# Optimization experiments

Hardware: AMD Instinct MI355X
Metric: run time of the kernel (lower is better)

## Reference

```python
import jax, jax.numpy as jnp
import numpy as np

NUM_HEADS = 12

def setup_inputs() -> dict:
    key = jax.random.key(0)
    ks = jax.random.split(key, 6)
    B, N, C, P = 16, 785, 768, 48
    return {
        "x": jax.random.normal(ks[0], (B, N, C), jnp.float32),
        "qkv_w": jax.random.normal(ks[1], (3 * C, C), jnp.float32) * 0.02,
        "pos_emb": jax.random.normal(ks[2], (N, N, P), jnp.float32) * 0.02,
        "pos_proj_w": jax.random.normal(ks[3], (NUM_HEADS, P), jnp.float32) * 0.02,
        "proj_w": jax.random.normal(ks[4], (C, C), jnp.float32) * 0.02,
        "proj_b": jnp.zeros((C,), jnp.float32),
    }

def reference(x, qkv_w, pos_emb, pos_proj_w, proj_w, proj_b):
    B, N, C = x.shape
    H = NUM_HEADS
    hd = C // H
    scale = hd ** -0.5
    # qkv projection: [B,N,3C] -> q,k,v each [B,H,N,hd]
    qkv = (x @ qkv_w.T).reshape(B, N, 3, H, hd)
    qkv = jnp.transpose(qkv, (2, 0, 3, 1, 4))
    q, k, v = qkv[0], qkv[1], qkv[2]
    # learned relative-position bias: [H,N,N]
    pos_score = jnp.einsum('nmp,hp->hnm', pos_emb, pos_proj_w)
    # attention scores: scale applied AFTER adding bias (matches original)
    attn = (jnp.einsum('bhnd,bhmd->bhnm', q, k) + pos_score[None]) * scale
    attn = jax.nn.softmax(attn, axis=-1)
    out = jnp.einsum('bhnm,bhmd->bhnd', attn, v)
    out = jnp.transpose(out, (0, 2, 1, 3)).reshape(B, N, C)
    return out @ proj_w.T + proj_b
```

## Files before the change

### kernel.cpp

```cpp
#include <hip/hip_runtime.h>
#include <hip/hip_fp16.h>

#define B_ 16
#define N_ 785
#define C_ 768
#define H_ 12
#define HD_ 64
#define P_ 48
#define M_ (B_*N_)
#define POSW 832
#define VTW  832
#define SLOG2E 0.1803368801111244f

#define OFF_Q   0
#define OFF_K   9646080
#define OFF_VT  19292160
#define OFF_POS 29515776
#define OFF_XF  37353216
#define OFF_AO  OFF_XF
#define OFF_WQ  47085312
#define OFF_WP  48854784

struct __align__(16) Half8 { __half h[8]; };
typedef _Float16 half8_t __attribute__((ext_vector_type(8)));
typedef _Float16 half4_t __attribute__((ext_vector_type(4)));
typedef float f32x4 __attribute__((ext_vector_type(4)));

__device__ __forceinline__ void gl16(const void* g, void* l) {
    __builtin_amdgcn_global_load_lds(
        (const __attribute__((address_space(1))) void*)g,
        (__attribute__((address_space(3))) void*)l, 16, 0, 0);
}

#define NX4 2411520
#define NQ4 442368
#define NP4 147456
#define NTOT4 (NX4+NQ4+NP4)

__global__ __launch_bounds__(256) void convert_f16(
    const float* __restrict__ x, const float* __restrict__ wq,
    const float* __restrict__ wp, _Float16* __restrict__ xo,
    _Float16* __restrict__ wqo, _Float16* __restrict__ wpo)
{
    int i = blockIdx.x * 256 + threadIdx.x;
    const float4* s; _Float16* d; int o;
    if (i < NX4)            { s = (const float4*)x;  d = xo;  o = i; }
    else if (i < NX4 + NQ4) { s = (const float4*)wq; d = wqo; o = i - NX4; }
    else                    { s = (const float4*)wp; d = wpo; o = i - NX4 - NQ4; }
    float4 v = s[o];
    half4_t h = { (_Float16)v.x, (_Float16)v.y, (_Float16)v.z, (_Float16)v.w };
    *(half4_t*)&d[o * 4] = h;
}

__global__ __launch_bounds__(256) void qkv_gemm_mfma(
    const _Float16* __restrict__ A, const _Float16* __restrict__ Bw,
    __half* __restrict__ qh, __half* __restrict__ kh, __half* __restrict__ vth)
{
    __shared__ _Float16 Asl[128 * 32];
    __shared__ _Float16 Bsl[128 * 32];

    const int t  = threadIdx.x;
    const int w  = t >> 6;
    const int l  = t & 63;
    const int lr = l & 15;
    const int lg = l >> 4;
    const int wm = (w >> 1) * 64;
    const int wn = (w & 1) * 64;
    const int n0 = blockIdx.x * 128;
    const int m0 = blockIdx.y * 128;

    const int f1 = t + 256;
    const int ar0 = t >> 2,  ac0 = (t & 3) * 8;
    const int ar1 = f1 >> 2, ac1 = (f1 & 3) * 8;
    const _Float16* Ag0 = A  + (size_t)(m0 + ar0) * 768 + ac0;
    const _Float16* Ag1 = A  + (size_t)(m0 + ar1) * 768 + ac1;
    const _Float16* Bg0 = Bw + (size_t)(n0 + ar0) * 768 + ac0;
    const _Float16* Bg1 = Bw + (size_t)(n0 + ar1) * 768 + ac1;
    _Float16* Al0 = &Asl[t * 8];
    _Float16* Al1 = &Asl[f1 * 8];
    _Float16* Bl0 = &Bsl[t * 8];
    _Float16* Bl1 = &Bsl[f1 * 8];

    f32x4 acc[4][4];
    #pragma unroll
    for (int i = 0; i < 4; ++i)
        #pragma unroll
        for (int j = 0; j < 4; ++j) acc[i][j] = (f32x4){0.f, 0.f, 0.f, 0.f};

    for (int k0 = 0; k0 < 768; k0 += 32) {
        gl16(Ag0 + k0, Al0); gl16(Ag1 + k0, Al1);
        gl16(Bg0 + k0, Bl0); gl16(Bg1 + k0, Bl1);
        __syncthreads();
        half8_t af[4], bf[4];
        #pragma unroll
        for (int i = 0; i < 4; ++i)
            af[i] = *(const half8_t*)&Asl[(wm + i * 16 + lr) * 32 + lg * 8];
        #pragma unroll
        for (int j = 0; j < 4; ++j)
            bf[j] = *(const half8_t*)&Bsl[(wn + j * 16 + lr) * 32 + lg * 8];
        __builtin_amdgcn_s_setprio(1);
        #pragma unroll
        for (int i = 0; i < 4; ++i)
            #pragma unroll
            for (int j = 0; j < 4; ++j)
                acc[i][j] = __builtin_amdgcn_mfma_f32_16x16x32_f16(af[i], bf[j], acc[i][j], 0, 0, 0);
        __builtin_amdgcn_s_setprio(0);
        __syncthreads();
    }

    const int tsel  = blockIdx.x / 6;
    const int nbase = n0 - tsel * 768;
    #pragma unroll
    for (int i = 0; i < 4; ++i) {
        #pragma unroll
        for (int r = 0; r < 4; ++r) {
            const int m = m0 + wm + i * 16 + lg * 4 + r;
            if (m >= M_) continue;
            const int bb = m / N_, nn = m - bb * N_;
            #pragma unroll
            for (int j = 0; j < 4; ++j) {
                const int nsec = nbase + wn + j * 16 + lr;
                const int hh = nsec >> 6, dd = nsec & 63;
                const float v = acc[i][j][r];
                if (tsel == 0)
                    qh[((size_t)(bb * H_ + hh) * N_ + nn) * HD_ + dd] = __float2half(v * SLOG2E);
                else if (tsel == 1)
                    kh[((size_t)(bb * H_ + hh) * N_ + nn) * HD_ + dd] = __float2half(v);
                else
                    vth[((size_t)(bb * H_ + hh) * HD_ + dd) * VTW + nn] = __float2half(v);
            }
        }
    }
}

__global__ __launch_bounds__(256) void pos_kernel(
    const float* __restrict__ pe, const float* __restrict__ pw,
    __half* __restrict__ posh)
{
    __shared__ float W[H_][P_];
    const int t = threadIdx.x;
    for (int i = t; i < H_ * P_; i += 256) W[i / P_][i % P_] = pw[i];
    __syncthreads();
    int nm = blockIdx.x * 256 + t;
    if (nm >= N_ * N_) return;
    float e[48];
    const float4* src = (const float4*)(pe + (size_t)nm * 48);
    #pragma unroll
    for (int i = 0; i < 12; ++i) {
        float4 v = src[i];
        e[4*i] = v.x; e[4*i+1] = v.y; e[4*i+2] = v.z; e[4*i+3] = v.w;
    }
    int n = nm / N_, m = nm - n * N_;
    #pragma unroll
    for (int hh = 0; hh < H_; ++hh) {
        float s = 0.f;
        #pragma unroll
        for (int p = 0; p < 48; ++p) s = fmaf(e[p], W[hh][p], s);
        posh[((size_t)hh * N_ + n) * POSW + m] = __float2half(s * SLOG2E);
    }
}

__global__ __launch_bounds__(256) void attn_mfma(
    const _Float16* __restrict__ qh, const _Float16* __restrict__ kh,
    const _Float16* __restrict__ vt, const _Float16* __restrict__ posh,
    _Float16* __restrict__ aoh)
{
    __shared__ _Float16 Kl[64][72];
    __shared__ _Float16 Vl[64][72];
    __shared__ _Float16 Bl[64][72];

    const int t  = threadIdx.x;
    const int w  = t >> 6;
    const int l  = t & 63;
    const int lr = l & 15;
    const int lg = l >> 4;

    const int g   = blockIdx.x;
    const int b   = g & 15;
    const int grp = g >> 4;
    const int qt  = grp / 12;
    const int h   = grp - qt * 12;
    const int bh  = b * H_ + h;
    const int n0  = qt * 64;

    const int qrow = n0 + w * 16 + lr;
    const int qrc  = qrow < N_ ? qrow : N_ - 1;
    const _Float16* qbase = qh + ((size_t)bh * N_ + qrc) * HD_;
    const half8_t qf0 = *(const half8_t*)(qbase + lg * 8);
    const half8_t qf1 = *(const half8_t*)(qbase + 32 + lg * 8);

    f32x4 O0 = {0.f,0.f,0.f,0.f}, O1 = O0, O2 = O0, O3 = O0;
    float m_run = -1e30f;
    float l_run = 0.f;

    const int srow = t >> 2;
    const int scol = (t & 3) * 16;
    const _Float16* kRow = kh + ((size_t)bh * N_) * HD_ + scol;
    const _Float16* vRow = vt + ((size_t)bh * HD_ + srow) * VTW + scol;
    const _Float16* bRow = posh + ((size_t)h * N_ + (n0 + srow < N_ ? n0 + srow : N_ - 1)) * POSW + scol;

    half8_t rk0, rk1, rv0, rv1, rb0, rb1;
    {
        const int gm = srow < N_ ? srow : N_ - 1;
        const half8_t* ks = (const half8_t*)(kRow + (size_t)gm * HD_);
        rk0 = ks[0]; rk1 = ks[1];
        const half8_t* vs = (const half8_t*)vRow;
        rv0 = vs[0]; rv1 = vs[1];
        const half8_t* bs = (const half8_t*)bRow;
        rb0 = bs[0]; rb1 = bs[1];
    }

    for (int c = 0; c < 13; ++c) {
        *(half8_t*)&Kl[srow][scol]     = rk0;
        *(half8_t*)&Kl[srow][scol + 8] = rk1;
        *(half8_t*)&Vl[srow][scol]     = rv0;
        *(half8_t*)&Vl[srow][scol + 8] = rv1;
        *(half8_t*)&Bl[srow][scol]     = rb0;
        *(half8_t*)&Bl[srow][scol + 8] = rb1;
        __syncthreads();

        if (c < 12) {
            const int m0n = (c + 1) * 64;
            const int gm  = (m0n + srow) < N_ ? (m0n + srow) : N_ - 1;
            const half8_t* ks = (const half8_t*)(kRow + (size_t)gm * HD_);
            rk0 = ks[0]; rk1 = ks[1];
            const half8_t* vs = (const half8_t*)(vRow + m0n);
            rv0 = vs[0]; rv1 = vs[1];
            const half8_t* bs = (const half8_t*)(bRow + m0n);
            rb0 = bs[0]; rb1 = bs[1];
        }

        f32x4 s[4];
        __builtin_amdgcn_s_setprio(1);
        #pragma unroll
        for (int ms = 0; ms < 4; ++ms) {
            half8_t k0 = *(const half8_t*)&Kl[ms * 16 + lr][lg * 8];
            half8_t k1 = *(const half8_t*)&Kl[ms * 16 + lr][32 + lg * 8];
            f32x4 acc = {0.f, 0.f, 0.f, 0.f};
            acc = __builtin_amdgcn_mfma_f32_16x16x32_f16(k0, qf0, acc, 0, 0, 0);
            acc = __builtin_amdgcn_mfma_f32_16x16x32_f16(k1, qf1, acc, 0, 0, 0);
            s[ms] = acc;
        }
        __builtin_amdgcn_s_setprio(0);

        #pragma unroll
        for (int ms = 0; ms < 4; ++ms) {
            half4_t b4 = *(const half4_t*)&Bl[w * 16 + lr][ms * 16 + lg * 4];
            s[ms][0] += (float)b4[0];
            s[ms][1] += (float)b4[1];
            s[ms][2] += (float)b4[2];
            s[ms][3] += (float)b4[3];
        }
        if (c == 12) {
            #pragma unroll
            for (int ms = 0; ms < 4; ++ms)
                #pragma unroll
                for (int r = 0; r < 4; ++r)
                    if (ms * 16 + lg * 4 + r >= 17) s[ms][r] = -1e30f;
        }

        float smax = fmaxf(fmaxf(fmaxf(s[0][0], s[0][1]), fmaxf(s[0][2], s[0][3])),
                           fmaxf(fmaxf(s[1][0], s[1][1]), fmaxf(s[1][2], s[1][3])));
        smax = fmaxf(smax, fmaxf(fmaxf(fmaxf(s[2][0], s[2][1]), fmaxf(s[2][2], s[2][3])),
                                 fmaxf(fmaxf(s[3][0], s[3][1]), fmaxf(s[3][2], s[3][3]))));
        smax = fmaxf(smax, __shfl_xor(smax, 16));
        smax = fmaxf(smax, __shfl_xor(smax, 32));

        if (__any(smax > m_run + 8.f)) {
            const float mn    = fmaxf(m_run, smax);
            const float alpha = exp2f(m_run - mn);
            m_run = mn;
            l_run *= alpha;
            const float a0 = __shfl(alpha, lg * 4 + 0);
            const float a1 = __shfl(alpha, lg * 4 + 1);
            const float a2 = __shfl(alpha, lg * 4 + 2);
            const float a3 = __shfl(alpha, lg * 4 + 3);
            O0[0]*=a0; O0[1]*=a1; O0[2]*=a2; O0[3]*=a3;
            O1[0]*=a0; O1[1]*=a1; O1[2]*=a2; O1[3]*=a3;
            O2[0]*=a0; O2[1]*=a1; O2[2]*=a2; O2[3]*=a3;
            O3[0]*=a0; O3[1]*=a1; O3[2]*=a2; O3[3]*=a3;
        }

        float p[4][4];
        float psum = 0.f;
        #pragma unroll
        for (int ms = 0; ms < 4; ++ms)
            #pragma unroll
            for (int r = 0; r < 4; ++r) {
                p[ms][r] = exp2f(s[ms][r] - m_run);
                psum += p[ms][r];
            }
        psum += __shfl_xor(psum, 16);
        psum += __shfl_xor(psum, 32);
        l_run += psum;

        half8_t pa0 = { (_Float16)p[0][0], (_Float16)p[0][1], (_Float16)p[0][2], (_Float16)p[0][3],
                        (_Float16)p[1][0], (_Float16)p[1][1], (_Float16)p[1][2], (_Float16)p[1][3] };
        half8_t pa1 = { (_Float16)p[2][0], (_Float16)p[2][1], (_Float16)p[2][2], (_Float16)p[2][3],
                        (_Float16)p[3][0], (_Float16)p[3][1], (_Float16)p[3][2], (_Float16)p[3][3] };

        __builtin_amdgcn_s_setprio(1);
        #pragma unroll
        for (int ds = 0; ds < 4; ++ds) {
            const _Float16* vr = &Vl[ds * 16 + lr][0];
            half4_t v00 = *(const half4_t*)&vr[lg * 4];
            half4_t v01 = *(const half4_t*)&vr[16 + lg * 4];
            half4_t v10 = *(const half4_t*)&vr[32 + lg * 4];
            half4_t v11 = *(const half4_t*)&vr[48 + lg * 4];
            half8_t vf0 = __builtin_shufflevector(v00, v01, 0, 1, 2, 3, 4, 5, 6, 7);
            half8_t vf1 = __builtin_shufflevector(v10, v11, 0, 1, 2, 3, 4, 5, 6, 7);
            f32x4& Od = (ds == 0 ? O0 : ds == 1 ? O1 : ds == 2 ? O2 : O3);
            Od = __builtin_amdgcn_mfma_f32_16x16x32_f16(pa0, vf0, Od, 0, 0, 0);
            Od = __builtin_amdgcn_mfma_f32_16x16x32_f16(pa1, vf1, Od, 0, 0, 0);
        }
        __builtin_amdgcn_s_setprio(0);
        __syncthreads();
    }

    const int bb = bh / H_;
    #pragma unroll
    for (int r = 0; r < 4; ++r) {
        const int n = n0 + w * 16 + lg * 4 + r;
        if (n >= N_) continue;
        const float lv  = __shfl(l_run, lg * 4 + r);
        const float inv = 1.f / lv;
        _Float16* dst = aoh + ((size_t)(bb * N_ + n)) * C_ + h * HD_;
        dst[0 * 16 + lr] = (_Float16)(O0[r] * inv);
        dst[1 * 16 + lr] = (_Float16)(O1[r] * inv);
        dst[2 * 16 + lr] = (_Float16)(O2[r] * inv);
        dst[3 * 16 + lr] = (_Float16)(O3[r] * inv);
    }
}

__global__ __launch_bounds__(256) void proj_gemm_mfma(
    const _Float16* __restrict__ A, const _Float16* __restrict__ Bw,
    const float* __restrict__ bias, float* __restrict__ out)
{
    __shared__ _Float16 Asl[128 * 32];
    __shared__ _Float16 Bsl[128 * 32];

    const int t  = threadIdx.x;
    const int w  = t >> 6;
    const int l  = t & 63;
    const int lr = l & 15;
    const int lg = l >> 4;
    const int wm = (w >> 1) * 64;
    const int wn = (w & 1) * 64;
    const int n0 = blockIdx.x * 128;
    const int m0 = blockIdx.y * 128;

    const int f1 = t + 256;
    const int ar0 = t >> 2,  ac0 = (t & 3) * 8;
    const int ar1 = f1 >> 2, ac1 = (f1 & 3) * 8;
    const _Float16* Ag0 = A  + (size_t)(m0 + ar0) * 768 + ac0;
    const _Float16* Ag1 = A  + (size_t)(m0 + ar1) * 768 + ac1;
    const _Float16* Bg0 = Bw + (size_t)(n0 + ar0) * 768 + ac0;
    const _Float16* Bg1 = Bw + (size_t)(n0 + ar1) * 768 + ac1;
    _Float16* Al0 = &Asl[t * 8];
    _Float16* Al1 = &Asl[f1 * 8];
    _Float16* Bl0 = &Bsl[t * 8];
    _Float16* Bl1 = &Bsl[f1 * 8];

    f32x4 acc[4][4];
    #pragma unroll
    for (int i = 0; i < 4; ++i)
        #pragma unroll
        for (int j = 0; j < 4; ++j) acc[i][j] = (f32x4){0.f, 0.f, 0.f, 0.f};

    for (int k0 = 0; k0 < 768; k0 += 32) {
        gl16(Ag0 + k0, Al0); gl16(Ag1 + k0, Al1);
        gl16(Bg0 + k0, Bl0); gl16(Bg1 + k0, Bl1);
        __syncthreads();
        half8_t af[4], bf[4];
        #pragma unroll
        for (int i = 0; i < 4; ++i)
            af[i] = *(const half8_t*)&Asl[(wm + i * 16 + lr) * 32 + lg * 8];
        #pragma unroll
        for (int j = 0; j < 4; ++j)
            bf[j] = *(const half8_t*)&Bsl[(wn + j * 16 + lr) * 32 + lg * 8];
        __builtin_amdgcn_s_setprio(1);
        #pragma unroll
        for (int i = 0; i < 4; ++i)
            #pragma unroll
            for (int j = 0; j < 4; ++j)
                acc[i][j] = __builtin_amdgcn_mfma_f32_16x16x32_f16(af[i], bf[j], acc[i][j], 0, 0, 0);
        __builtin_amdgcn_s_setprio(0);
        __syncthreads();
    }

    float bj[4];
    #pragma unroll
    for (int j = 0; j < 4; ++j) bj[j] = bias[n0 + wn + j * 16 + lr];
    #pragma unroll
    for (int i = 0; i < 4; ++i) {
        #pragma unroll
        for (int r = 0; r < 4; ++r) {
            const int m = m0 + wm + i * 16 + lg * 4 + r;
            if (m >= M_) continue;
            #pragma unroll
            for (int j = 0; j < 4; ++j) {
                const int n = n0 + wn + j * 16 + lr;
                out[(size_t)m * 768 + n] = acc[i][j][r] + bj[j];
            }
        }
    }
}

extern "C" void kernel_launch(void* const* d_in, const int* in_sizes, int n_in,
                              void* d_out, int out_size, void* d_ws, size_t ws_size,
                              hipStream_t stream)
{
    const float* x     = (const float*)d_in[0];
    const float* qkv_w = (const float*)d_in[1];
    const float* pe    = (const float*)d_in[2];
    const float* pw    = (const float*)d_in[3];
    const float* pjw   = (const float*)d_in[4];
    const float* pjb   = (const float*)d_in[5];
    float* out = (float*)d_out;

    _Float16* wsh  = (_Float16*)d_ws;
    _Float16* qh   = wsh + OFF_Q;
    _Float16* kh   = wsh + OFF_K;
    _Float16* vth  = wsh + OFF_VT;
    _Float16* posh = wsh + OFF_POS;
    _Float16* xf   = wsh + OFF_XF;
    _Float16* aoh  = wsh + OFF_AO;
    _Float16* wqf  = wsh + OFF_WQ;
    _Float16* wpf  = wsh + OFF_WP;

    convert_f16<<<dim3(NTOT4 / 256), 256, 0, stream>>>(x, qkv_w, pjw, xf, wqf, wpf);
    qkv_gemm_mfma<<<dim3(18, 99), 256, 0, stream>>>(
        xf, wqf, (__half*)qh, (__half*)kh, (__half*)vth);
    pos_kernel<<<dim3((N_ * N_ + 255) / 256), 256, 0, stream>>>(pe, pw, (__half*)posh);
    attn_mfma<<<dim3(13 * 12 * 16), 256, 0, stream>>>(qh, kh, vth, posh, aoh);
    proj_gemm_mfma<<<dim3(6, 99), 256, 0, stream>>>(aoh, wpf, pjb, out);
}
```

Before: 290.6 us.

## Double-buffer GEMM LDS tiles and remap workgroups across XCDs

Both the QKV and projection GEMMs now use two LDS buffers, so the next K-slice is fetched with global_load_lds while MFMAs run on the current one. This removes one barrier per iteration and hides load latency. The 2D grids are flattened to 1D, and a swizzle maps consecutive logical tiles onto the same XCD so tiles sharing A and B rows are more likely to hit the same L2. The cost is twice the LDS per block, which may lower occupancy. These GEMMs are only part of the total time, next to the attention kernel.

Result: faster. 270.1 us (-7.1%).

```diff
diff --git a/kernel.cpp b/kernel.cpp
--- a/kernel.cpp
+++ b/kernel.cpp
@@ -32,6 +32,13 @@
         (__attribute__((address_space(3))) void*)l, 16, 0, 0);
 }
 
+__device__ __forceinline__ int xcd_swz(int o, int nwg) {
+    const int q = nwg >> 3, r = nwg & 7;
+    const int xcd = o & 7, idx = o >> 3;
+    const int base = xcd < r ? xcd * (q + 1) : r * (q + 1) + (xcd - r) * q;
+    return base + idx;
+}
+
 #define NX4 2411520
 #define NQ4 442368
 #define NP4 147456
@@ -52,12 +59,14 @@
     *(half4_t*)&d[o * 4] = h;
 }
 
+#define QKV_NWG (18 * 99)
+
 __global__ __launch_bounds__(256) void qkv_gemm_mfma(
     const _Float16* __restrict__ A, const _Float16* __restrict__ Bw,
     __half* __restrict__ qh, __half* __restrict__ kh, __half* __restrict__ vth)
 {
-    __shared__ _Float16 Asl[128 * 32];
-    __shared__ _Float16 Bsl[128 * 32];
+    __shared__ _Float16 Asl[2][128 * 32];
+    __shared__ _Float16 Bsl[2][128 * 32];
 
     const int t  = threadIdx.x;
     const int w  = t >> 6;
@@ -66,8 +75,11 @@
     const int lg = l >> 4;
     const int wm = (w >> 1) * 64;
     const int wn = (w & 1) * 64;
-    const int n0 = blockIdx.x * 128;
-    const int m0 = blockIdx.y * 128;
+
+    const int g  = xcd_swz(blockIdx.x, QKV_NWG);
+    const int nt = g % 18;
+    const int n0 = nt * 128;
+    const int m0 = (g / 18) * 128;
 
     const int f1 = t + 256;
     const int ar0 = t >> 2,  ac0 = (t & 3) * 8;
@@ -76,10 +88,6 @@
     const _Float16* Ag1 = A  + (size_t)(m0 + ar1) * 768 + ac1;
     const _Float16* Bg0 = Bw + (size_t)(n0 + ar0) * 768 + ac0;
     const _Float16* Bg1 = Bw + (size_t)(n0 + ar1) * 768 + ac1;
-    _Float16* Al0 = &Asl[t * 8];
-    _Float16* Al1 = &Asl[f1 * 8];
-    _Float16* Bl0 = &Bsl[t * 8];
-    _Float16* Bl1 = &Bsl[f1 * 8];
 
     f32x4 acc[4][4];
     #pragma unroll
@@ -87,17 +95,25 @@
         #pragma unroll
         for (int j = 0; j < 4; ++j) acc[i][j] = (f32x4){0.f, 0.f, 0.f, 0.f};
 
-    for (int k0 = 0; k0 < 768; k0 += 32) {
-        gl16(Ag0 + k0, Al0); gl16(Ag1 + k0, Al1);
-        gl16(Bg0 + k0, Bl0); gl16(Bg1 + k0, Bl1);
-        __syncthreads();
+    gl16(Ag0, &Asl[0][t * 8]); gl16(Ag1, &Asl[0][f1 * 8]);
+    gl16(Bg0, &Bsl[0][t * 8]); gl16(Bg1, &Bsl[0][f1 * 8]);
+    __syncthreads();
+
+    #pragma unroll 2
+    for (int it = 0; it < 24; ++it) {
+        const int cur = it & 1;
+        if (it < 23) {
+            const int kn = (it + 1) * 32;
+            gl16(Ag0 + kn, &Asl[cur ^ 1][t * 8]); gl16(Ag1 + kn, &Asl[cur ^ 1][f1 * 8]);
+            gl16(Bg0 + kn, &Bsl[cur ^ 1][t * 8]); gl16(Bg1 + kn, &Bsl[cur ^ 1][f1 * 8]);
+        }
         half8_t af[4], bf[4];
         #pragma unroll
         for (int i = 0; i < 4; ++i)
-            af[i] = *(const half8_t*)&Asl[(wm + i * 16 + lr) * 32 + lg * 8];
+            af[i] = *(const half8_t*)&Asl[cur][(wm + i * 16 + lr) * 32 + lg * 8];
         #pragma unroll
         for (int j = 0; j < 4; ++j)
-            bf[j] = *(const half8_t*)&Bsl[(wn + j * 16 + lr) * 32 + lg * 8];
+            bf[j] = *(const half8_t*)&Bsl[cur][(wn + j * 16 + lr) * 32 + lg * 8];
         __builtin_amdgcn_s_setprio(1);
         #pragma unroll
         for (int i = 0; i < 4; ++i)
@@ -108,7 +124,7 @@
         __syncthreads();
     }
 
-    const int tsel  = blockIdx.x / 6;
+    const int tsel  = nt / 6;
     const int nbase = n0 - tsel * 768;
     #pragma unroll
     for (int i = 0; i < 4; ++i) {
@@ -332,12 +348,14 @@
     }
 }
 
+#define PROJ_NWG (6 * 99)
+
 __global__ __launch_bounds__(256) void proj_gemm_mfma(
     const _Float16* __restrict__ A, const _Float16* __restrict__ Bw,
     const float* __restrict__ bias, float* __restrict__ out)
 {
-    __shared__ _Float16 Asl[128 * 32];
-    __shared__ _Float16 Bsl[128 * 32];
+    __shared__ _Float16 Asl[2][128 * 32];
+    __shared__ _Float16 Bsl[2][128 * 32];
 
     const int t  = threadIdx.x;
     const int w  = t >> 6;
@@ -346,8 +364,10 @@
     const int lg = l >> 4;
     const int wm = (w >> 1) * 64;
     const int wn = (w & 1) * 64;
-    const int n0 = blockIdx.x * 128;
-    const int m0 = blockIdx.y * 128;
+
+    const int g  = xcd_swz(blockIdx.x, PROJ_NWG);
+    const int n0 = (g % 6) * 128;
+    const int m0 = (g / 6) * 128;
 
     const int f1 = t + 256;
     const int ar0 = t >> 2,  ac0 = (t & 3) * 8;
@@ -356,10 +376,6 @@
     const _Float16* Ag1 = A  + (size_t)(m0 + ar1) * 768 + ac1;
     const _Float16* Bg0 = Bw + (size_t)(n0 + ar0) * 768 + ac0;
     const _Float16* Bg1 = Bw + (size_t)(n0 + ar1) * 768 + ac1;
-    _Float16* Al0 = &Asl[t * 8];
-    _Float16* Al1 = &Asl[f1 * 8];
-    _Float16* Bl0 = &Bsl[t * 8];
-    _Float16* Bl1 = &Bsl[f1 * 8];
 
     f32x4 acc[4][4];
     #pragma unroll
@@ -367,17 +383,25 @@
         #pragma unroll
         for (int j = 0; j < 4; ++j) acc[i][j] = (f32x4){0.f, 0.f, 0.f, 0.f};
 
-    for (int k0 = 0; k0 < 768; k0 += 32) {
-        gl16(Ag0 + k0, Al0); gl16(Ag1 + k0, Al1);
-        gl16(Bg0 + k0, Bl0); gl16(Bg1 + k0, Bl1);
-        __syncthreads();
+    gl16(Ag0, &Asl[0][t * 8]); gl16(Ag1, &Asl[0][f1 * 8]);
+    gl16(Bg0, &Bsl[0][t * 8]); gl16(Bg1, &Bsl[0][f1 * 8]);
+    __syncthreads();
+
+    #pragma unroll 2
+    for (int it = 0; it < 24; ++it) {
+        const int cur = it & 1;
+        if (it < 23) {
+            const int kn = (it + 1) * 32;
+            gl16(Ag0 + kn, &Asl[cur ^ 1][t * 8]); gl16(Ag1 + kn, &Asl[cur ^ 1][f1 * 8]);
+            gl16(Bg0 + kn, &Bsl[cur ^ 1][t * 8]); gl16(Bg1 + kn, &Bsl[cur ^ 1][f1 * 8]);
+        }
         half8_t af[4], bf[4];
         #pragma unroll
         for (int i = 0; i < 4; ++i)
-            af[i] = *(const half8_t*)&Asl[(wm + i * 16 + lr) * 32 + lg * 8];
+            af[i] = *(const half8_t*)&Asl[cur][(wm + i * 16 + lr) * 32 + lg * 8];
         #pragma unroll
         for (int j = 0; j < 4; ++j)
-            bf[j] = *(const half8_t*)&Bsl[(wn + j * 16 + lr) * 32 + lg * 8];
+            bf[j] = *(const half8_t*)&Bsl[cur][(wn + j * 16 + lr) * 32 + lg * 8];
         __builtin_amdgcn_s_setprio(1);
         #pragma unroll
         for (int i = 0; i < 4; ++i)
@@ -429,9 +453,9 @@
     _Float16* wpf  = wsh + OFF_WP;
 
     convert_f16<<<dim3(NTOT4 / 256), 256, 0, stream>>>(x, qkv_w, pjw, xf, wqf, wpf);
-    qkv_gemm_mfma<<<dim3(18, 99), 256, 0, stream>>>(
+    qkv_gemm_mfma<<<dim3(QKV_NWG), 256, 0, stream>>>(
         xf, wqf, (__half*)qh, (__half*)kh, (__half*)vth);
     pos_kernel<<<dim3((N_ * N_ + 255) / 256), 256, 0, stream>>>(pe, pw, (__half*)posh);
     attn_mfma<<<dim3(13 * 12 * 16), 256, 0, stream>>>(qh, kh, vth, posh, aoh);
-    proj_gemm_mfma<<<dim3(6, 99), 256, 0, stream>>>(aoh, wpf, pjb, out);
-}
+    proj_gemm_mfma<<<dim3(PROJ_NWG), 256, 0, stream>>>(aoh, wpf, pjb, out);
+}
```
